# Performance work log

Measured on AMD Instinct MI355X. Metric: run time of the kernel, lower is better.

Reference implementation:

```python
import jax, jax.numpy as jnp
import numpy as np

WD = 11
HF = WD // 2  # 5

def _offsets():
    # Reproduce the torch module's expanding-ring offset ordering exactly.
    offs = []
    for i in range(1, HF + 1):
        for v in range(HF - i, HF + i + 1):
            for u in range(HF - i, HF + i + 1):
                if not (u == HF and v == HF) and (u, v) not in offs:
                    offs.append((u, v))
    return offs  # length WD*WD-1 = 120

_OFFS = _offsets()


def setup_inputs() -> dict:
    key = jax.random.key(0)
    x = jax.random.normal(key, (2, 3, 384, 1280), dtype=jnp.float32)
    return {"x": x, "attack": 1}


def reference(x, attack):
    n, c, h, w = x.shape
    xm = jnp.mean(x, axis=1)  # [n,h,w] grayscale
    xp = jnp.pad(xm, ((0, 0), (HF, HF), (HF, HF)), mode="reflect")  # [n,h+2*HF,w+2*HF]
    # All 120 shifted views in ring order; static slices, stacked on channel dim.
    shifted = jnp.stack([xp[:, v:v + h, u:u + w] for (u, v) in _OFFS], axis=1)  # [n,120,h,w]
    center = xm[:, None, :, :]
    if attack:
        return jax.nn.sigmoid((shifted - center) * 100000.0)
    return shifted >= center
```

## Files before the change

kernel.cpp:

```cpp
#include <hip/hip_runtime.h>
#include <cstddef>
#include <cstdint>

constexpr int N_  = 2;
constexpr int C_  = 3;
constexpr int H_  = 384;
constexpr int W_  = 1280;
constexpr int HWp = H_ * W_;
constexpr int NOFF = 120;
constexpr int HF_  = 5;

struct OffTab { int du[NOFF]; int dv[NOFF]; };
constexpr OffTab make_offs() {
    OffTab t{};
    int idx = 0;
    for (int i = 1; i <= HF_; ++i)
        for (int v = HF_ - i; v <= HF_ + i; ++v)
            for (int u = HF_ - i; u <= HF_ + i; ++u) {
                if (u == HF_ && v == HF_) continue;
                int au = u < HF_ ? HF_ - u : u - HF_;
                int av = v < HF_ ? HF_ - v : v - HF_;
                int r = au > av ? au : av;
                if (r != i) continue;
                t.du[idx] = u - HF_;
                t.dv[idx] = v - HF_;
                ++idx;
            }
    return t;
}
__constant__ OffTab OFFS = make_offs();

__global__ __launch_bounds__(256) void mean_kernel(const float* __restrict__ x,
                                                   float* __restrict__ xm) {
    int i = blockIdx.x * 256 + threadIdx.x;
    constexpr int TOT4 = N_ * HWp / 4;
    if (i >= TOT4) return;
    int n = i / (HWp / 4);
    int j = i - n * (HWp / 4);
    const float4* x0 = (const float4*)(x + (size_t)n * C_ * HWp);
    const float4* x1 = (const float4*)(x + (size_t)n * C_ * HWp + HWp);
    const float4* x2 = (const float4*)(x + (size_t)n * C_ * HWp + 2 * HWp);
    float4 a = x0[j], b = x1[j], c = x2[j];
    float4 m;
    m.x = (a.x + b.x + c.x) / 3.0f;
    m.y = (a.y + b.y + c.y) / 3.0f;
    m.z = (a.z + b.z + c.z) / 3.0f;
    m.w = (a.w + b.w + c.w) / 3.0f;
    ((float4*)xm)[i] = m;
}

__device__ __forceinline__ float sig1e5(float d) {
    float e = __expf(d * -100000.0f);
    return __builtin_amdgcn_rcpf(1.0f + e);
}

__global__ __launch_bounds__(320) void census_rows(const float* __restrict__ xm,
                                                   float* __restrict__ out) {
    int b  = blockIdx.x;
    int y  = b % H_;
    int t2 = b / H_;
    int k  = t2 % NOFF;
    int n  = t2 / NOFF;

    int du = OFFS.du[k];
    int dv = OFFS.dv[k];
    int yy = y + dv;
    yy = yy < 0 ? -yy : yy;
    yy = yy >= H_ ? 2 * (H_ - 1) - yy : yy;

    const float* cr = xm + (size_t)n * HWp + (size_t)y  * W_;
    const float* sr = xm + (size_t)n * HWp + (size_t)yy * W_;

    int x4 = (int)threadIdx.x * 4;
    float4 c = *(const float4*)(cr + x4);
    float cc[4] = {c.x, c.y, c.z, c.w};

    float s[4];
#pragma unroll
    for (int j = 0; j < 4; ++j) {
        int xx = x4 + j + du;
        xx = xx < 0 ? -xx : xx;
        xx = xx >= W_ ? 2 * (W_ - 1) - xx : xx;
        s[j] = sr[xx];
    }

    float d[4], r[4];
    bool slow = false;
#pragma unroll
    for (int j = 0; j < 4; ++j) {
        d[j] = s[j] - cc[j];
        r[j] = d[j] > 0.0f ? 1.0f : 0.0f;
        slow |= (fabsf(d[j]) < 1.6e-4f);
    }
    if (__builtin_expect(slow, 0)) {
#pragma unroll
        for (int j = 0; j < 4; ++j) r[j] = sig1e5(d[j]);
    }

    float4 o; o.x = r[0]; o.y = r[1]; o.z = r[2]; o.w = r[3];
    *(float4*)(out + (size_t)n * NOFF * HWp + (size_t)k * HWp
               + (size_t)y * W_ + x4) = o;
}

__device__ __forceinline__ float mean3(const float* __restrict__ xn, int off) {
    return (xn[off] + xn[off + HWp] + xn[off + 2 * HWp]) / 3.0f;
}

__global__ __launch_bounds__(320) void census_rows_fused(const float* __restrict__ x,
                                                         float* __restrict__ out) {
    int b  = blockIdx.x;
    int y  = b % H_;
    int t2 = b / H_;
    int k  = t2 % NOFF;
    int n  = t2 / NOFF;

    int du = OFFS.du[k];
    int dv = OFFS.dv[k];
    int yy = y + dv;
    yy = yy < 0 ? -yy : yy;
    yy = yy >= H_ ? 2 * (H_ - 1) - yy : yy;

    const float* xn = x + (size_t)n * C_ * HWp;
    int x4 = (int)threadIdx.x * 4;

    float cc[4], s[4];
#pragma unroll
    for (int j = 0; j < 4; ++j) cc[j] = mean3(xn, y * W_ + x4 + j);
#pragma unroll
    for (int j = 0; j < 4; ++j) {
        int xx = x4 + j + du;
        xx = xx < 0 ? -xx : xx;
        xx = xx >= W_ ? 2 * (W_ - 1) - xx : xx;
        s[j] = mean3(xn, yy * W_ + xx);
    }

    float d[4], r[4];
    bool slow = false;
#pragma unroll
    for (int j = 0; j < 4; ++j) {
        d[j] = s[j] - cc[j];
        r[j] = d[j] > 0.0f ? 1.0f : 0.0f;
        slow |= (fabsf(d[j]) < 1.6e-4f);
    }
    if (__builtin_expect(slow, 0)) {
#pragma unroll
        for (int j = 0; j < 4; ++j) r[j] = sig1e5(d[j]);
    }

    float4 o; o.x = r[0]; o.y = r[1]; o.z = r[2]; o.w = r[3];
    *(float4*)(out + (size_t)n * NOFF * HWp + (size_t)k * HWp
               + (size_t)y * W_ + x4) = o;
}

extern "C" void kernel_launch(void* const* d_in, const int* in_sizes, int n_in,
                              void* d_out, int out_size, void* d_ws, size_t ws_size,
                              hipStream_t stream) {
    const float* x = (const float*)d_in[0];
    float* out = (float*)d_out;

    const size_t xm_bytes = (size_t)N_ * HWp * sizeof(float);
    const int census_blocks = N_ * NOFF * H_;

    if (ws_size >= xm_bytes) {
        float* xm = (float*)d_ws;
        const int mean_blocks = (N_ * HWp / 4 + 255) / 256;
        mean_kernel<<<mean_blocks, 256, 0, stream>>>(x, xm);
        census_rows<<<census_blocks, 320, 0, stream>>>(xm, out);
    } else {
        census_rows_fused<<<census_blocks, 320, 0, stream>>>(x, out);
    }
}
```

Measured before the change: 513.9 us.

## Process output planes in row segments per block with nontemporal stores

```diff
diff --git a/kernel.cpp b/kernel.cpp
--- a/kernel.cpp
+++ b/kernel.cpp
@@ -9,6 +9,8 @@
 constexpr int HWp = H_ * W_;
 constexpr int NOFF = 120;
 constexpr int HF_  = 5;
+
+typedef float vfloat4 __attribute__((ext_vector_type(4)));
 
 struct OffTab { int du[NOFF]; int dv[NOFF]; };
 constexpr OffTab make_offs() {
@@ -54,102 +56,113 @@
     return __builtin_amdgcn_rcpf(1.0f + e);
 }
 
-__global__ __launch_bounds__(320) void census_rows(const float* __restrict__ xm,
-                                                   float* __restrict__ out) {
-    int b  = blockIdx.x;
-    int y  = b % H_;
-    int t2 = b / H_;
-    int k  = t2 % NOFF;
-    int n  = t2 / NOFF;
+__device__ __forceinline__ int reflect(int i, int n) {
+    i = i < 0 ? -i : i;
+    i = i >= n ? 2 * (n - 1) - i : i;
+    return i;
+}
+
+constexpr int SEG = 8;
+constexpr int RS  = H_ / SEG;
+
+__global__ __launch_bounds__(320) void census_planes(const float* __restrict__ xm,
+                                                     float* __restrict__ out) {
+    int b   = blockIdx.x;
+    int n   = b & 1;
+    int t2  = b >> 1;
+    int seg = t2 % SEG;
+    int k   = t2 / SEG;
 
     int du = OFFS.du[k];
     int dv = OFFS.dv[k];
-    int yy = y + dv;
-    yy = yy < 0 ? -yy : yy;
-    yy = yy >= H_ ? 2 * (H_ - 1) - yy : yy;
-
-    const float* cr = xm + (size_t)n * HWp + (size_t)y  * W_;
-    const float* sr = xm + (size_t)n * HWp + (size_t)yy * W_;
 
     int x4 = (int)threadIdx.x * 4;
-    float4 c = *(const float4*)(cr + x4);
-    float cc[4] = {c.x, c.y, c.z, c.w};
+    int xr[4];
+#pragma unroll
+    for (int j = 0; j < 4; ++j) xr[j] = reflect(x4 + j + du, W_);
 
-    float s[4];
+    const float* xmn = xm + (size_t)n * HWp;
+    float* outp = out + (size_t)n * NOFF * HWp + (size_t)k * HWp + x4;
+
+    int y0 = seg * RS;
+#pragma unroll 2
+    for (int y = y0; y < y0 + RS; ++y) {
+        int yy = reflect(y + dv, H_);
+        const float* cr = xmn + (size_t)y  * W_;
+        const float* sr = xmn + (size_t)yy * W_;
+
+        float4 c = *(const float4*)(cr + x4);
+        float cc[4] = {c.x, c.y, c.z, c.w};
+
+        float s[4];
 #pragma unroll
-    for (int j = 0; j < 4; ++j) {
-        int xx = x4 + j + du;
-        xx = xx < 0 ? -xx : xx;
-        xx = xx >= W_ ? 2 * (W_ - 1) - xx : xx;
-        s[j] = sr[xx];
+        for (int j = 0; j < 4; ++j) s[j] = sr[xr[j]];
+
+        float r[4];
+        bool slow = false;
+#pragma unroll
+        for (int j = 0; j < 4; ++j) {
+            float d = s[j] - cc[j];
+            r[j] = d > 0.0f ? 1.0f : 0.0f;
+            slow |= (fabsf(d) < 1.6e-4f);
+        }
+        if (__builtin_expect(slow, 0)) {
+#pragma unroll
+            for (int j = 0; j < 4; ++j) r[j] = sig1e5(s[j] - cc[j]);
+        }
+        vfloat4 o = {r[0], r[1], r[2], r[3]};
+        __builtin_nontemporal_store(o, (vfloat4*)(outp + (size_t)y * W_));
     }
-
-    float d[4], r[4];
-    bool slow = false;
-#pragma unroll
-    for (int j = 0; j < 4; ++j) {
-        d[j] = s[j] - cc[j];
-        r[j] = d[j] > 0.0f ? 1.0f : 0.0f;
-        slow |= (fabsf(d[j]) < 1.6e-4f);
-    }
-    if (__builtin_expect(slow, 0)) {
-#pragma unroll
-        for (int j = 0; j < 4; ++j) r[j] = sig1e5(d[j]);
-    }
-
-    float4 o; o.x = r[0]; o.y = r[1]; o.z = r[2]; o.w = r[3];
-    *(float4*)(out + (size_t)n * NOFF * HWp + (size_t)k * HWp
-               + (size_t)y * W_ + x4) = o;
 }
 
 __device__ __forceinline__ float mean3(const float* __restrict__ xn, int off) {
     return (xn[off] + xn[off + HWp] + xn[off + 2 * HWp]) / 3.0f;
 }
 
-__global__ __launch_bounds__(320) void census_rows_fused(const float* __restrict__ x,
-                                                         float* __restrict__ out) {
-    int b  = blockIdx.x;
-    int y  = b % H_;
-    int t2 = b / H_;
-    int k  = t2 % NOFF;
-    int n  = t2 / NOFF;
+__global__ __launch_bounds__(320) void census_planes_fused(const float* __restrict__ x,
+                                                           float* __restrict__ out) {
+    int b   = blockIdx.x;
+    int n   = b & 1;
+    int t2  = b >> 1;
+    int seg = t2 % SEG;
+    int k   = t2 / SEG;
 
     int du = OFFS.du[k];
     int dv = OFFS.dv[k];
-    int yy = y + dv;
-    yy = yy < 0 ? -yy : yy;
-    yy = yy >= H_ ? 2 * (H_ - 1) - yy : yy;
+
+    int x4 = (int)threadIdx.x * 4;
+    int xr[4];
+#pragma unroll
+    for (int j = 0; j < 4; ++j) xr[j] = reflect(x4 + j + du, W_);
 
     const float* xn = x + (size_t)n * C_ * HWp;
-    int x4 = (int)threadIdx.x * 4;
+    float* outp = out + (size_t)n * NOFF * HWp + (size_t)k * HWp + x4;
 
-    float cc[4], s[4];
+    int y0 = seg * RS;
+    for (int y = y0; y < y0 + RS; ++y) {
+        int yy = reflect(y + dv, H_);
+
+        float cc[4], s[4];
 #pragma unroll
-    for (int j = 0; j < 4; ++j) cc[j] = mean3(xn, y * W_ + x4 + j);
+        for (int j = 0; j < 4; ++j) cc[j] = mean3(xn, y * W_ + x4 + j);
 #pragma unroll
-    for (int j = 0; j < 4; ++j) {
-        int xx = x4 + j + du;
-        xx = xx < 0 ? -xx : xx;
-        xx = xx >= W_ ? 2 * (W_ - 1) - xx : xx;
-        s[j] = mean3(xn, yy * W_ + xx);
+        for (int j = 0; j < 4; ++j) s[j]  = mean3(xn, yy * W_ + xr[j]);
+
+        float r[4];
+        bool slow = false;
+#pragma unroll
+        for (int j = 0; j < 4; ++j) {
+            float d = s[j] - cc[j];
+            r[j] = d > 0.0f ? 1.0f : 0.0f;
+            slow |= (fabsf(d) < 1.6e-4f);
+        }
+        if (__builtin_expect(slow, 0)) {
+#pragma unroll
+            for (int j = 0; j < 4; ++j) r[j] = sig1e5(s[j] - cc[j]);
+        }
+        vfloat4 o = {r[0], r[1], r[2], r[3]};
+        __builtin_nontemporal_store(o, (vfloat4*)(outp + (size_t)y * W_));
     }
-
-    float d[4], r[4];
-    bool slow = false;
-#pragma unroll
-    for (int j = 0; j < 4; ++j) {
-        d[j] = s[j] - cc[j];
-        r[j] = d[j] > 0.0f ? 1.0f : 0.0f;
-        slow |= (fabsf(d[j]) < 1.6e-4f);
-    }
-    if (__builtin_expect(slow, 0)) {
-#pragma unroll
-        for (int j = 0; j < 4; ++j) r[j] = sig1e5(d[j]);
-    }
-
-    float4 o; o.x = r[0]; o.y = r[1]; o.z = r[2]; o.w = r[3];
-    *(float4*)(out + (size_t)n * NOFF * HWp + (size_t)k * HWp
-               + (size_t)y * W_ + x4) = o;
 }
 
 extern "C" void kernel_launch(void* const* d_in, const int* in_sizes, int n_in,
@@ -159,14 +172,14 @@
     float* out = (float*)d_out;
 
     const size_t xm_bytes = (size_t)N_ * HWp * sizeof(float);
-    const int census_blocks = N_ * NOFF * H_;
+    const int census_blocks = N_ * NOFF * SEG;
 
     if (ws_size >= xm_bytes) {
         float* xm = (float*)d_ws;
         const int mean_blocks = (N_ * HWp / 4 + 255) / 256;
         mean_kernel<<<mean_blocks, 256, 0, stream>>>(x, xm);
-        census_rows<<<census_blocks, 320, 0, stream>>>(xm, out);
+        census_planes<<<census_blocks, 320, 0, stream>>>(xm, out);
     } else {
-        census_rows_fused<<<census_blocks, 320, 0, stream>>>(x, out);
+        census_planes_fused<<<census_blocks, 320, 0, stream>>>(x, out);
     }
 }
```

New measurement: 516.6 us. About the same (+0.5%).
